# Optimization experiments

Hardware: AMD Instinct MI355X
Metric: run time of the kernel (lower is better)

The kernel has to match this reference:

```python
import jax, jax.numpy as jnp
import numpy as np


def setup_inputs() -> dict:
    key = jax.random.key(0)
    k1, k2 = jax.random.split(key)
    z = jax.random.normal(k1, (16, 1024, 512), dtype=jnp.float32)
    codebook = jax.random.normal(k2, (2048, 64), dtype=jnp.float32)
    return {"z": z, "codebook": codebook}


def reference(z, codebook):
    """VQQuantizer.forward: group latent, euclidean nearest-codebook quantize,
    straight-through estimator, commit loss = mse(stop_grad(z_q), z).
    Returns (codes, indices, commit_loss) matching dict values
    {'codes','indices','commit_loss'} ('z' and 'state' are z_grouped / codes).
    """
    D = codebook.shape[1]            # codebook_dim
    shp = z.shape                    # [B, T, latent]
    zg = z.reshape(shp[:-1] + (-1, D))   # [B, T, G, D]
    zf = zg.reshape(-1, D)               # [N, D], N = B*T*G
    # squared euclidean distances: ||z||^2 - 2 z.c + ||c||^2  -> [N, K]
    dist = (
        jnp.sum(zf * zf, axis=1, keepdims=True)
        - 2.0 * (zf @ codebook.T)
        + jnp.sum(codebook * codebook, axis=1)
    )
    idx = jnp.argmin(dist, axis=-1)      # [N]
    zq = codebook[idx].reshape(zg.shape)  # [B, T, G, D]
    commit_loss = jnp.mean((jax.lax.stop_gradient(zq) - zg) ** 2)
    # straight-through
    zq_st = zg + jax.lax.stop_gradient(zq - zg)
    codes = zq_st.reshape(shp)            # [B, T, latent]
    indices = idx.reshape(zg.shape[:-1])  # [B, T, G]
    return codes, indices, commit_loss
```

## Files before the change

### kernel.cpp

```cpp
#include <hip/hip_runtime.h>

typedef short s16x8 __attribute__((ext_vector_type(8)));
typedef float f32x4 __attribute__((ext_vector_type(4)));

#define CODES_ELEMS 8388608
#define N_ROWS      131072
#define IDX_OFF     CODES_ELEMS
#define LOSS_OFF    (CODES_ELEMS + N_ROWS)

#define WS_LOSS 0
#define WS_CC   64
#define WS_CBS  8448
#define MARGIN_T 0.0625f
#define DIST_OFF 512.0f

__device__ __forceinline__ float bf2f(unsigned short h) { return __uint_as_float(((unsigned)h) << 16); }
__device__ __forceinline__ unsigned short f2bf(float f) {
  unsigned u = __float_as_uint(f);
  u += 0x7fffu + ((u >> 16) & 1u);
  return (unsigned short)(u >> 16);
}
__device__ __forceinline__ void gl_lds16(const void* g, void* l) {
  __builtin_amdgcn_global_load_lds(
      (__attribute__((address_space(1))) void*)(g),
      (__attribute__((address_space(3))) void*)(l), 16, 0, 0);
}

__global__ __launch_bounds__(256) void vq_prep(const float* __restrict__ cb,
                                               float* __restrict__ cc,
                                               unsigned short* __restrict__ cbs,
                                               float* __restrict__ loss) {
  int t = threadIdx.x;
  if (blockIdx.x == 0 && t == 0) loss[0] = 0.f;
  int e = blockIdx.x * 256 + t;
  int k = e >> 7, K = e & 127;
  int s = K >> 5, rem = K & 31, q = rem >> 3, j = rem & 7;
  int d = (s < 2) ? K : (K - 64);
  float c = cb[k * 64 + d];
  unsigned short c1 = f2bf(c);
  unsigned short val = (s < 2) ? c1 : f2bf(c - bf2f(c1));
  int chunk = k >> 6, ct = (k >> 4) & 3, n = k & 15;
  cbs[(((size_t)(chunk * 4 + s) * 4 + ct) * 64 + (q * 16 + n)) * 8 + j] = val;
  float sq = c * c;
  #pragma unroll
  for (int m = 1; m < 64; m <<= 1) sq += __shfl_xor(sq, m, 64);
  if ((t & 63) == 0) cc[k] = sq;
}

__global__ __launch_bounds__(256) void VQQuantizer_30064771072206_kernel(
    const float* __restrict__ zf, const float* __restrict__ cb,
    const unsigned short* __restrict__ cbs, const float* __restrict__ cc,
    float* __restrict__ loss, float* __restrict__ out)
{
  __shared__ __align__(16) unsigned short bt[2][8192];
  __shared__ __align__(16) float cc_l[2048];
  int*   idx_l  = (int*)&bt[0][0];
  int*   flg    = (int*)((char*)&bt[0][0] + 1024);
  int*   nf     = (int*)((char*)&bt[0][0] + 2048);
  float (*zl)[68] = (float(*)[68])((char*)&bt[0][0] + 2064);
  float* zz_l   = (float*)((char*)&bt[0][0] + 4240);
  int*   rows_s = (int*)((char*)&bt[0][0] + 4272);
  float (*rv)[8] = (float(*)[8])((char*)&bt[0][0] + 4304);
  int   (*ri)[8] = (int(*)[8])((char*)&bt[0][0] + 4432);
  float* wsum   = (float*)((char*)&bt[0][0] + 4560);

  const int t = threadIdx.x, w = t >> 6, l = t & 63;
  const int col = l & 15, q = l >> 4;
  const int R0 = blockIdx.x * 256;
  const float4* zf4 = (const float4*)zf;
  const float4* cb4 = (const float4*)cb;

  #pragma unroll
  for (int i = 0; i < 4; ++i) {
    int s0 = i * 256 + w * 64;
    gl_lds16(cbs + (size_t)(s0 + l) * 8, &bt[0][(size_t)s0 * 8]);
  }
  #pragma unroll
  for (int i = 0; i < 2; ++i)
    ((float4*)cc_l)[i * 256 + t] = ((const float4*)cc)[i * 256 + t];

  s16x8 az1[4][2], az2[4][2];
  #pragma unroll
  for (int tile = 0; tile < 4; ++tile) {
    int row = R0 + tile * 64 + 16 * w + col;
    const float4* zr = zf4 + (size_t)row * 16;
    #pragma unroll
    for (int s = 0; s < 2; ++s) {
      float4 u0 = zr[s * 8 + q * 2];
      float4 u1 = zr[s * 8 + q * 2 + 1];
      float m2[8] = {-2.f*u0.x, -2.f*u0.y, -2.f*u0.z, -2.f*u0.w,
                     -2.f*u1.x, -2.f*u1.y, -2.f*u1.z, -2.f*u1.w};
      #pragma unroll
      for (int j = 0; j < 8; ++j) {
        unsigned short h1 = f2bf(m2[j]);
        unsigned short h2 = f2bf(m2[j] - bf2f(h1));
        az1[tile][s][j] = (short)h1;
        az2[tile][s][j] = (short)h2;
      }
    }
  }

  unsigned p1[4][4], p2[4][4];
  #pragma unroll
  for (int tile = 0; tile < 4; ++tile)
    #pragma unroll
    for (int r = 0; r < 4; ++r) { p1[tile][r] = 0xFFFFFFFFu; p2[tile][r] = 0xFFFFFFFFu; }

  __syncthreads();

  int cur = 0;
  for (int chunk = 0; chunk < 32; ++chunk) {
    if (chunk + 1 < 32) {
      const unsigned short* src = cbs + (size_t)(chunk + 1) * 8192;
      unsigned short* dst = &bt[cur ^ 1][0];
      #pragma unroll
      for (int i = 0; i < 4; ++i) {
        int s0 = i * 256 + w * 64;
        gl_lds16(src + (size_t)(s0 + l) * 8, dst + (size_t)s0 * 8);
      }
    }
    const unsigned short* bb = &bt[cur][l * 8];
    const float* ccc = &cc_l[chunk * 64 + col];
    #pragma unroll
    for (int ct = 0; ct < 4; ++ct) {
      float nh = DIST_OFF + ccc[ct * 16];
      const unsigned short* base = bb + ct * 512;
      s16x8 b0 = *(const s16x8*)(base + 0 * 2048);
      s16x8 b1 = *(const s16x8*)(base + 1 * 2048);
      s16x8 b2 = *(const s16x8*)(base + 2 * 2048);
      s16x8 b3 = *(const s16x8*)(base + 3 * 2048);
      unsigned pid = (unsigned)(chunk * 4 + ct);
      #pragma unroll
      for (int tile = 0; tile < 4; ++tile) {
        f32x4 acc; acc[0] = nh; acc[1] = nh; acc[2] = nh; acc[3] = nh;
        acc = __builtin_amdgcn_mfma_f32_16x16x32_bf16(az1[tile][0], b0, acc, 0, 0, 0);
        acc = __builtin_amdgcn_mfma_f32_16x16x32_bf16(az1[tile][1], b1, acc, 0, 0, 0);
        acc = __builtin_amdgcn_mfma_f32_16x16x32_bf16(az1[tile][0], b2, acc, 0, 0, 0);
        acc = __builtin_amdgcn_mfma_f32_16x16x32_bf16(az1[tile][1], b3, acc, 0, 0, 0);
        acc = __builtin_amdgcn_mfma_f32_16x16x32_bf16(az2[tile][0], b0, acc, 0, 0, 0);
        acc = __builtin_amdgcn_mfma_f32_16x16x32_bf16(az2[tile][1], b1, acc, 0, 0, 0);
        #pragma unroll
        for (int r = 0; r < 4; ++r) {
          unsigned pd = (__float_as_uint(acc[r]) & 0xFFFFFF80u) | pid;
          unsigned mx = p1[tile][r] > pd ? p1[tile][r] : pd;
          p2[tile][r] = p2[tile][r] < mx ? p2[tile][r] : mx;
          p1[tile][r] = p1[tile][r] < pd ? p1[tile][r] : pd;
        }
      }
    }
    __syncthreads();
    cur ^= 1;
  }

  if (t == 0) *nf = 0;
  __syncthreads();
  #pragma unroll
  for (int tile = 0; tile < 4; ++tile) {
    #pragma unroll
    for (int r = 0; r < 4; ++r) {
      float a   = __uint_as_float(p1[tile][r] & 0xFFFFFF80u);
      int   ia  = (int)(p1[tile][r] & 127u) * 16 + col;
      float b2v = __uint_as_float(p2[tile][r] & 0xFFFFFF80u);
      #pragma unroll
      for (int m = 1; m < 16; m <<= 1) {
        float oa = __shfl_xor(a, m, 64);
        int   oi = __shfl_xor(ia, m, 64);
        float ob = __shfl_xor(b2v, m, 64);
        float hv = fmaxf(a, oa);
        b2v = fminf(fminf(b2v, ob), hv);
        bool take = (oa < a) || (oa == a && oi < ia);
        a = take ? oa : a; ia = take ? oi : ia;
      }
      if (col == 0) {
        int rl = tile * 64 + 16 * w + q * 4 + r;
        idx_l[rl] = ia;
        if (b2v - a < MARGIN_T) {
          int p = atomicAdd(nf, 1);
          flg[p] = rl;
        }
      }
    }
  }
  __syncthreads();

  int count = *nf;
  for (int itb = 0; itb * 8 < count; ++itb) {
    if (itb) __syncthreads();
    if (t < 8) {
      int ii = itb * 8 + t;
      rows_s[t] = flg[ii < count ? ii : count - 1];
    }
    __syncthreads();
    if (t < 128) {
      int r = t >> 4, dq = t & 15;
      *(float4*)&zl[r][dq * 4] = zf4[(size_t)(R0 + rows_s[r]) * 16 + dq];
    }
    __syncthreads();
    if (t < 8) {
      float s = 0.f;
      for (int d = 0; d < 64; ++d) { float v = zl[t][d]; s += v * v; }
      zz_l[t] = s;
    }
    __syncthreads();

    float bv[8]; int bi[8];
    #pragma unroll
    for (int r = 0; r < 8; ++r) { bv[r] = 3.402823466e38f; bi[r] = 0; }
    #pragma unroll 1
    for (int o = 0; o < 8; ++o) {
      int c = o * 256 + t;
      const float4* cr = cb4 + (size_t)c * 16;
      float a[8];
      #pragma unroll
      for (int r = 0; r < 8; ++r) a[r] = 0.f;
      #pragma unroll 4
      for (int dq = 0; dq < 16; ++dq) {
        float4 cv = cr[dq];
        #pragma unroll
        for (int r = 0; r < 8; ++r) {
          float4 z4 = *(const float4*)&zl[r][dq * 4];
          a[r] += z4.x * cv.x;
          a[r] += z4.y * cv.y;
          a[r] += z4.z * cv.z;
          a[r] += z4.w * cv.w;
        }
      }
      float ccv = cc_l[c];
      #pragma unroll
      for (int r = 0; r < 8; ++r) {
        float t0 = zz_l[r] - 2.0f * a[r];
        float dist = t0 + ccv;
        if (dist < bv[r]) { bv[r] = dist; bi[r] = c; }
      }
    }
    #pragma unroll
    for (int r = 0; r < 8; ++r) {
      float v = bv[r]; int idx = bi[r];
      #pragma unroll
      for (int m = 1; m < 64; m <<= 1) {
        float ov = __shfl_xor(v, m, 64); int oi = __shfl_xor(idx, m, 64);
        if (ov < v || (ov == v && oi < idx)) { v = ov; idx = oi; }
      }
      if (l == 0) { rv[w][r] = v; ri[w][r] = idx; }
    }
    __syncthreads();
    if (t < 8) {
      float fv = rv[0][t]; int fi = ri[0][t];
      #pragma unroll
      for (int k = 1; k < 4; ++k) {
        if (rv[k][t] < fv || (rv[k][t] == fv && ri[k][t] < fi)) { fv = rv[k][t]; fi = ri[k][t]; }
      }
      idx_l[rows_s[t]] = fi;
    }
  }
  __syncthreads();

  float4* out4 = (float4*)out;
  float lsum = 0.f;
  #pragma unroll 2
  for (int i = 0; i < 16; ++i) {
    int f = i * 256 + t;
    int row = f >> 4, dq = f & 15;
    int k = idx_l[row];
    float4 qv = cb4[(size_t)k * 16 + dq];
    float4 zv = zf4[(size_t)(R0 + row) * 16 + dq];
    float dx = qv.x - zv.x, dy = qv.y - zv.y, dz = qv.z - zv.z, dw = qv.w - zv.w;
    float4 st; st.x = zv.x + dx; st.y = zv.y + dy; st.z = zv.z + dz; st.w = zv.w + dw;
    out4[(size_t)(R0 + row) * 16 + dq] = st;
    lsum += dx * dx; lsum += dy * dy; lsum += dz * dz; lsum += dw * dw;
  }
  out[IDX_OFF + R0 + t] = (float)idx_l[t];
  #pragma unroll
  for (int m = 1; m < 64; m <<= 1) lsum += __shfl_xor(lsum, m, 64);
  if (l == 0) wsum[w] = lsum;
  __syncthreads();
  if (t == 0) atomicAdd(loss, wsum[0] + wsum[1] + wsum[2] + wsum[3]);
}

__global__ void vq_finalize(const float* __restrict__ loss, float* __restrict__ out) {
  out[LOSS_OFF] = loss[0] * (1.f / 8388608.f);
}

extern "C" void kernel_launch(void* const* d_in, const int* in_sizes, int n_in,
                              void* d_out, int out_size, void* d_ws, size_t ws_size,
                              hipStream_t stream) {
  const float* z  = (const float*)d_in[0];
  const float* cb = (const float*)d_in[1];
  float* out = (float*)d_out;
  float* loss = (float*)((char*)d_ws + WS_LOSS);
  float* cc   = (float*)((char*)d_ws + WS_CC);
  unsigned short* cbs = (unsigned short*)((char*)d_ws + WS_CBS);

  vq_prep<<<1024, 256, 0, stream>>>(cb, cc, cbs, loss);
  VQQuantizer_30064771072206_kernel<<<512, 256, 0, stream>>>(z, cb, cbs, cc, loss, out);
  vq_finalize<<<1, 1, 0, stream>>>(loss, out);
}
```

Measured before the change: 240.7 us.

## Split codebook search across two blocks per row tile with last-arriver merge

Each 256-row tile is now processed by two blocks, each scanning half of the codebook chunks, which doubles the grid from 512 to 1024 blocks. Each half writes its per-row best, index and second-best into scratch space in the output buffer. A global atomic counter picks the second finisher, which merges both halves, flags ambiguous rows and runs the fp32 fallback and the epilogue. The aim is better occupancy and CU utilisation on the MFMA-bound search. The cost is extra global traffic, threadfence synchronisation, and reuse of the output region as scratch before it is overwritten.

```diff
diff --git a/kernel.cpp b/kernel.cpp
--- a/kernel.cpp
+++ b/kernel.cpp
@@ -11,6 +11,7 @@
 #define WS_LOSS 0
 #define WS_CC   64
 #define WS_CBS  8448
+#define WS_DONE 532736
 #define MARGIN_T 0.0625f
 #define DIST_OFF 512.0f
 
@@ -29,9 +30,11 @@
 __global__ __launch_bounds__(256) void vq_prep(const float* __restrict__ cb,
                                                float* __restrict__ cc,
                                                unsigned short* __restrict__ cbs,
-                                               float* __restrict__ loss) {
+                                               float* __restrict__ loss,
+                                               int* __restrict__ done) {
   int t = threadIdx.x;
   if (blockIdx.x == 0 && t == 0) loss[0] = 0.f;
+  if (blockIdx.x < 2) done[blockIdx.x * 256 + t] = 0;
   int e = blockIdx.x * 256 + t;
   int k = e >> 7, K = e & 127;
   int s = K >> 5, rem = K & 31, q = rem >> 3, j = rem & 7;
@@ -50,7 +53,7 @@
 __global__ __launch_bounds__(256) void VQQuantizer_30064771072206_kernel(
     const float* __restrict__ zf, const float* __restrict__ cb,
     const unsigned short* __restrict__ cbs, const float* __restrict__ cc,
-    float* __restrict__ loss, float* __restrict__ out)
+    float* __restrict__ loss, int* __restrict__ done, float* __restrict__ out)
 {
   __shared__ __align__(16) unsigned short bt[2][8192];
   __shared__ __align__(16) float cc_l[2048];
@@ -63,17 +66,21 @@
   float (*rv)[8] = (float(*)[8])((char*)&bt[0][0] + 4304);
   int   (*ri)[8] = (int(*)[8])((char*)&bt[0][0] + 4432);
   float* wsum   = (float*)((char*)&bt[0][0] + 4560);
+  int*   secondp= (int*)((char*)&bt[0][0] + 4576);
 
   const int t = threadIdx.x, w = t >> 6, l = t & 63;
   const int col = l & 15, q = l >> 4;
-  const int R0 = blockIdx.x * 256;
+  const int pair = blockIdx.x & 511, h = blockIdx.x >> 9;
+  const int R0 = pair * 256;
+  const int C0 = h * 16;
   const float4* zf4 = (const float4*)zf;
   const float4* cb4 = (const float4*)cb;
+  unsigned* sc = (unsigned*)(out + (size_t)pair * 16384);
 
   #pragma unroll
   for (int i = 0; i < 4; ++i) {
     int s0 = i * 256 + w * 64;
-    gl_lds16(cbs + (size_t)(s0 + l) * 8, &bt[0][(size_t)s0 * 8]);
+    gl_lds16(cbs + (size_t)C0 * 8192 + (size_t)(s0 + l) * 8, &bt[0][(size_t)s0 * 8]);
   }
   #pragma unroll
   for (int i = 0; i < 2; ++i)
@@ -109,9 +116,10 @@
   __syncthreads();
 
   int cur = 0;
-  for (int chunk = 0; chunk < 32; ++chunk) {
-    if (chunk + 1 < 32) {
-      const unsigned short* src = cbs + (size_t)(chunk + 1) * 8192;
+  for (int c = 0; c < 16; ++c) {
+    int gchunk = C0 + c;
+    if (c + 1 < 16) {
+      const unsigned short* src = cbs + (size_t)(gchunk + 1) * 8192;
       unsigned short* dst = &bt[cur ^ 1][0];
       #pragma unroll
       for (int i = 0; i < 4; ++i) {
@@ -120,7 +128,7 @@
       }
     }
     const unsigned short* bb = &bt[cur][l * 8];
-    const float* ccc = &cc_l[chunk * 64 + col];
+    const float* ccc = &cc_l[gchunk * 64 + col];
     #pragma unroll
     for (int ct = 0; ct < 4; ++ct) {
       float nh = DIST_OFF + ccc[ct * 16];
@@ -129,7 +137,7 @@
       s16x8 b1 = *(const s16x8*)(base + 1 * 2048);
       s16x8 b2 = *(const s16x8*)(base + 2 * 2048);
       s16x8 b3 = *(const s16x8*)(base + 3 * 2048);
-      unsigned pid = (unsigned)(chunk * 4 + ct);
+      unsigned pid = (unsigned)(gchunk * 4 + ct);
       #pragma unroll
       for (int tile = 0; tile < 4; ++tile) {
         f32x4 acc; acc[0] = nh; acc[1] = nh; acc[2] = nh; acc[3] = nh;
@@ -152,8 +160,6 @@
     cur ^= 1;
   }
 
-  if (t == 0) *nf = 0;
-  __syncthreads();
   #pragma unroll
   for (int tile = 0; tile < 4; ++tile) {
     #pragma unroll
@@ -173,12 +179,34 @@
       }
       if (col == 0) {
         int rl = tile * 64 + 16 * w + q * 4 + r;
-        idx_l[rl] = ia;
-        if (b2v - a < MARGIN_T) {
-          int p = atomicAdd(nf, 1);
-          flg[p] = rl;
-        }
-      }
+        unsigned* s = sc + rl * 6 + h * 3;
+        s[0] = __float_as_uint(a);
+        s[1] = (unsigned)ia;
+        s[2] = __float_as_uint(b2v);
+      }
+    }
+  }
+  __threadfence();
+  if (t == 0) *secondp = (atomicAdd(&done[pair], 1) == 1) ? 1 : 0;
+  __syncthreads();
+  if (!*secondp) return;
+  __threadfence();
+
+  if (t == 0) *nf = 0;
+  __syncthreads();
+  {
+    unsigned a0b = sc[t * 6 + 0], c0b = sc[t * 6 + 1], s0b = sc[t * 6 + 2];
+    unsigned a1b = sc[t * 6 + 3], c1b = sc[t * 6 + 4], s1b = sc[t * 6 + 5];
+    float a0 = __uint_as_float(a0b), a1 = __uint_as_float(a1b);
+    float s0 = __uint_as_float(s0b), s1 = __uint_as_float(s1b);
+    bool take1 = (a1 < a0) || (a1 == a0 && (int)c1b < (int)c0b);
+    float best = take1 ? a1 : a0;
+    int   bi   = take1 ? (int)c1b : (int)c0b;
+    float sec  = fminf(fminf(s0, s1), fmaxf(a0, a1));
+    idx_l[t] = bi;
+    if (sec - best < MARGIN_T) {
+      int p_ = atomicAdd(nf, 1);
+      flg[p_] = t;
     }
   }
   __syncthreads();
@@ -203,9 +231,9 @@
     }
     __syncthreads();
 
-    float bv[8]; int bi[8];
-    #pragma unroll
-    for (int r = 0; r < 8; ++r) { bv[r] = 3.402823466e38f; bi[r] = 0; }
+    float bv[8]; int bi2[8];
+    #pragma unroll
+    for (int r = 0; r < 8; ++r) { bv[r] = 3.402823466e38f; bi2[r] = 0; }
     #pragma unroll 1
     for (int o = 0; o < 8; ++o) {
       int c = o * 256 + t;
@@ -230,12 +258,12 @@
       for (int r = 0; r < 8; ++r) {
         float t0 = zz_l[r] - 2.0f * a[r];
         float dist = t0 + ccv;
-        if (dist < bv[r]) { bv[r] = dist; bi[r] = c; }
+        if (dist < bv[r]) { bv[r] = dist; bi2[r] = c; }
       }
     }
     #pragma unroll
     for (int r = 0; r < 8; ++r) {
-      float v = bv[r]; int idx = bi[r];
+      float v = bv[r]; int idx = bi2[r];
       #pragma unroll
       for (int m = 1; m < 64; m <<= 1) {
         float ov = __shfl_xor(v, m, 64); int oi = __shfl_xor(idx, m, 64);
@@ -290,8 +318,9 @@
   float* loss = (float*)((char*)d_ws + WS_LOSS);
   float* cc   = (float*)((char*)d_ws + WS_CC);
   unsigned short* cbs = (unsigned short*)((char*)d_ws + WS_CBS);
-
-  vq_prep<<<1024, 256, 0, stream>>>(cb, cc, cbs, loss);
-  VQQuantizer_30064771072206_kernel<<<512, 256, 0, stream>>>(z, cb, cbs, cc, loss, out);
+  int*   done = (int*)((char*)d_ws + WS_DONE);
+
+  vq_prep<<<1024, 256, 0, stream>>>(cb, cc, cbs, loss, done);
+  VQQuantizer_30064771072206_kernel<<<1024, 256, 0, stream>>>(z, cb, cbs, cc, loss, done, out);
   vq_finalize<<<1, 1, 0, stream>>>(loss, out);
 }
```

Measured after the change: 364.3 us. 1.51x slower.

## Load codebook fragments directly from global instead of LDS double buffer

Applied to the files above, without the earlier changes.

Removes the LDS double-buffered staging of the split-bf16 codebook and the per-chunk barrier, so each lane reads its MFMA B fragments straight from global memory (through L1/L2), with partial unrolling of the ct loop. Scratch shared arrays become separate declarations instead of aliasing the staging buffer. This drops the barriers and LDS traffic and cuts LDS usage, which may raise occupancy. In exchange, global load latency is now exposed directly in the MFMA loop with no explicit prefetch, and all four waves issue redundant loads of the same data.

```diff
diff --git a/kernel.cpp b/kernel.cpp
--- a/kernel.cpp
+++ b/kernel.cpp
@@ -19,11 +19,6 @@
   unsigned u = __float_as_uint(f);
   u += 0x7fffu + ((u >> 16) & 1u);
   return (unsigned short)(u >> 16);
-}
-__device__ __forceinline__ void gl_lds16(const void* g, void* l) {
-  __builtin_amdgcn_global_load_lds(
-      (__attribute__((address_space(1))) void*)(g),
-      (__attribute__((address_space(3))) void*)(l), 16, 0, 0);
 }
 
 __global__ __launch_bounds__(256) void vq_prep(const float* __restrict__ cb,
@@ -52,17 +47,16 @@
     const unsigned short* __restrict__ cbs, const float* __restrict__ cc,
     float* __restrict__ loss, float* __restrict__ out)
 {
-  __shared__ __align__(16) unsigned short bt[2][8192];
   __shared__ __align__(16) float cc_l[2048];
-  int*   idx_l  = (int*)&bt[0][0];
-  int*   flg    = (int*)((char*)&bt[0][0] + 1024);
-  int*   nf     = (int*)((char*)&bt[0][0] + 2048);
-  float (*zl)[68] = (float(*)[68])((char*)&bt[0][0] + 2064);
-  float* zz_l   = (float*)((char*)&bt[0][0] + 4240);
-  int*   rows_s = (int*)((char*)&bt[0][0] + 4272);
-  float (*rv)[8] = (float(*)[8])((char*)&bt[0][0] + 4304);
-  int   (*ri)[8] = (int(*)[8])((char*)&bt[0][0] + 4432);
-  float* wsum   = (float*)((char*)&bt[0][0] + 4560);
+  __shared__ int   idx_l[256];
+  __shared__ int   flg[256];
+  __shared__ int   nf;
+  __shared__ __align__(16) float zl[8][68];
+  __shared__ float zz_l[8];
+  __shared__ int   rows_s[8];
+  __shared__ float rv[4][8];
+  __shared__ int   ri[4][8];
+  __shared__ float wsum[4];
 
   const int t = threadIdx.x, w = t >> 6, l = t & 63;
   const int col = l & 15, q = l >> 4;
@@ -71,11 +65,6 @@
   const float4* cb4 = (const float4*)cb;
 
   #pragma unroll
-  for (int i = 0; i < 4; ++i) {
-    int s0 = i * 256 + w * 64;
-    gl_lds16(cbs + (size_t)(s0 + l) * 8, &bt[0][(size_t)s0 * 8]);
-  }
-  #pragma unroll
   for (int i = 0; i < 2; ++i)
     ((float4*)cc_l)[i * 256 + t] = ((const float4*)cc)[i * 256 + t];
 
@@ -108,23 +97,14 @@
 
   __syncthreads();
 
-  int cur = 0;
+  #pragma unroll 1
   for (int chunk = 0; chunk < 32; ++chunk) {
-    if (chunk + 1 < 32) {
-      const unsigned short* src = cbs + (size_t)(chunk + 1) * 8192;
-      unsigned short* dst = &bt[cur ^ 1][0];
-      #pragma unroll
-      for (int i = 0; i < 4; ++i) {
-        int s0 = i * 256 + w * 64;
-        gl_lds16(src + (size_t)(s0 + l) * 8, dst + (size_t)s0 * 8);
-      }
-    }
-    const unsigned short* bb = &bt[cur][l * 8];
+    const unsigned short* gb = cbs + (size_t)chunk * 8192 + (size_t)l * 8;
     const float* ccc = &cc_l[chunk * 64 + col];
-    #pragma unroll
+    #pragma unroll 2
     for (int ct = 0; ct < 4; ++ct) {
       float nh = DIST_OFF + ccc[ct * 16];
-      const unsigned short* base = bb + ct * 512;
+      const unsigned short* base = gb + ct * 512;
       s16x8 b0 = *(const s16x8*)(base + 0 * 2048);
       s16x8 b1 = *(const s16x8*)(base + 1 * 2048);
       s16x8 b2 = *(const s16x8*)(base + 2 * 2048);
@@ -148,11 +128,9 @@
         }
       }
     }
-    __syncthreads();
-    cur ^= 1;
-  }
-
-  if (t == 0) *nf = 0;
+  }
+
+  if (t == 0) nf = 0;
   __syncthreads();
   #pragma unroll
   for (int tile = 0; tile < 4; ++tile) {
@@ -175,7 +153,7 @@
         int rl = tile * 64 + 16 * w + q * 4 + r;
         idx_l[rl] = ia;
         if (b2v - a < MARGIN_T) {
-          int p = atomicAdd(nf, 1);
+          int p = atomicAdd(&nf, 1);
           flg[p] = rl;
         }
       }
@@ -183,7 +161,7 @@
   }
   __syncthreads();
 
-  int count = *nf;
+  int count = nf;
   for (int itb = 0; itb * 8 < count; ++itb) {
     if (itb) __syncthreads();
     if (t < 8) {
```

Result: slower. 247.1 us (+2.7%).
